# Kernel tuning notes

Measured on AMD Instinct MI355X. Metric: run time of the kernel, lower is better.

## Reference

```python
import jax, jax.numpy as jnp
import numpy as np

N, F, H, C, E = 100000, 128, 128, 40, 1600000


def setup_inputs() -> dict:
    key = jax.random.key(0)
    ks = jax.random.split(key, 8)
    x = jax.random.normal(ks[0], (N, F), dtype=jnp.float32)
    edge_index = jax.random.randint(ks[1], (2, E), 0, N, dtype=jnp.int64)
    s = 0.05
    return {
        "x": x,
        "edge_index": edge_index,
        "eps1": jnp.float32(0.0),
        "w1": jax.random.normal(ks[2], (F, H), dtype=jnp.float32) * s,
        "b1": jnp.zeros((H,), jnp.float32),
        "w2": jax.random.normal(ks[3], (H, H), dtype=jnp.float32) * s,
        "b2": jnp.zeros((H,), jnp.float32),
        "eps2": jnp.float32(0.0),
        "w3": jax.random.normal(ks[4], (H, H), dtype=jnp.float32) * s,
        "b3": jnp.zeros((H,), jnp.float32),
        "w4": jax.random.normal(ks[5], (H, C), dtype=jnp.float32) * s,
        "b4": jnp.zeros((C,), jnp.float32),
    }


def _gin_aggregate(h, src, dst, eps, n):
    # sum_{j -> i} h_j  +  (1+eps) * h_i
    agg = jax.ops.segment_sum(h[src], dst, num_segments=n)
    return (1.0 + eps) * h + agg


def reference(x, edge_index, eps1, w1, b1, w2, b2, eps2, w3, b3, w4, b4):
    src, dst = edge_index[0], edge_index[1]
    n = x.shape[0]
    # conv1: GINConv with MLP = Lin-ReLU-Lin-ReLU
    h = _gin_aggregate(x, src, dst, eps1, n)
    h = jax.nn.relu(h @ w1 + b1)
    h = jax.nn.relu(h @ w2 + b2)
    h = jax.nn.relu(h)  # outer F.relu (idempotent, kept for faithfulness)
    # dropout: identity in eval mode
    # conv2: GINConv with MLP = Lin-ReLU-Lin
    h2 = _gin_aggregate(h, src, dst, eps2, n)
    h2 = jax.nn.relu(h2 @ w3 + b3)
    h2 = h2 @ w4 + b4
    return jax.nn.log_softmax(h2, axis=1)
```

## Files before the change

kernel.cpp:

```cpp
#include <hip/hip_runtime.h>
#include <hip/hip_fp16.h>
#include <math.h>

constexpr int F = 128;
constexpr int C = 40;
constexpr int LDH = 136;
constexpr int BSHIFT = 8;
constexpr int BSIZE = 1 << BSHIFT;
constexpr int CHUNK = 8192;

typedef __attribute__((ext_vector_type(8))) _Float16 half8;
typedef __attribute__((ext_vector_type(4))) float float4v;


__global__ __launch_bounds__(256) void coarse_hist_kernel(const int* __restrict__ dst, int E, int NB,
                                                          int* __restrict__ coarse_count) {
    __shared__ int hist[512];
    int t = threadIdx.x;
    int c0 = blockIdx.x * CHUNK;
    int cend = min(c0 + CHUNK, E);
    for (int i = t; i < NB; i += 256) hist[i] = 0;
    __syncthreads();
    for (int i = c0 + t; i < cend; i += 256)
        atomicAdd(&hist[dst[i] >> BSHIFT], 1);
    __syncthreads();
    for (int i = t; i < NB; i += 256)
        if (hist[i]) atomicAdd(&coarse_count[i], hist[i]);
}

__global__ __launch_bounds__(512) void coarse_scan_kernel(const int* __restrict__ coarse_count,
                                                          int NB, int E,
                                                          int* __restrict__ coarse_start,
                                                          int* __restrict__ bucket_pos,
                                                          int* __restrict__ row_start, int N) {
    __shared__ int tmp[512];
    int t = threadIdx.x;
    int v = (t < NB) ? coarse_count[t] : 0;
    tmp[t] = v;
    __syncthreads();
    for (int d = 1; d < 512; d <<= 1) {
        int add = (t >= d) ? tmp[t - d] : 0;
        __syncthreads();
        tmp[t] += add;
        __syncthreads();
    }
    if (t < NB) {
        int ex = tmp[t] - v;
        coarse_start[t] = ex;
        bucket_pos[t] = ex;
    }
    if (t == 0) {
        coarse_start[NB] = E;
        row_start[N] = E;
    }
}

__global__ __launch_bounds__(256) void bucket_scatter_a_kernel(
        const int* __restrict__ src, const int* __restrict__ dst, int E, int NB,
        int* __restrict__ bucket_pos, unsigned* __restrict__ pairs) {
    __shared__ int hist[512];
    __shared__ int base[512];
    int t = threadIdx.x;
    int c0 = blockIdx.x * CHUNK;
    int cend = min(c0 + CHUNK, E);
    for (int i = t; i < NB; i += 256) hist[i] = 0;
    __syncthreads();
    for (int i = c0 + t; i < cend; i += 256)
        atomicAdd(&hist[dst[i] >> BSHIFT], 1);
    __syncthreads();
    for (int i = t; i < NB; i += 256) {
        int h = hist[i];
        base[i] = (h > 0) ? atomicAdd(&bucket_pos[i], h) : 0;
        hist[i] = 0;
    }
    __syncthreads();
    for (int i = c0 + t; i < cend; i += 256) {
        int d = dst[i];
        int b = d >> BSHIFT;
        int p = base[b] + atomicAdd(&hist[b], 1);
        pairs[p] = ((unsigned)(d & (BSIZE - 1)) << 24) | (unsigned)src[i];
    }
}

__global__ __launch_bounds__(256) void bucket_sort_kernel(const unsigned* __restrict__ pairs,
                                                          const int* __restrict__ coarse_start,
                                                          int N, int* __restrict__ row_start,
                                                          int* __restrict__ src_sorted) {
    __shared__ int hist[256];
    __shared__ int tmp[256];
    int b = blockIdx.x, t = threadIdx.x;
    int base = b << BSHIFT;
    int start = coarse_start[b];
    int end = coarse_start[b + 1];
    hist[t] = 0;
    __syncthreads();
    for (int i = start + t; i < end; i += 256)
        atomicAdd(&hist[pairs[i] >> 24], 1);
    __syncthreads();
    int v = hist[t];
    tmp[t] = v;
    __syncthreads();
    for (int d = 1; d < 256; d <<= 1) {
        int add = (t >= d) ? tmp[t - d] : 0;
        __syncthreads();
        tmp[t] += add;
        __syncthreads();
    }
    int ex = start + tmp[t] - v;
    if (base + t < N) row_start[base + t] = ex;
    hist[t] = ex;
    __syncthreads();
    for (int i = start + t; i < end; i += 256) {
        unsigned u = pairs[i];
        int p = atomicAdd(&hist[u >> 24], 1);
        src_sorted[p] = (int)(u & 0x00FFFFFFu);
    }
}


__global__ void conv_f16_kernel(const float* __restrict__ in, __half* __restrict__ out, int n4,
                                int* __restrict__ coarse_count, int NB) {
    int i = blockIdx.x * blockDim.x + threadIdx.x;
    if (blockIdx.x == 0) {
        for (int j = threadIdx.x; j < NB; j += 256) coarse_count[j] = 0;
    }
    if (i >= n4) return;
    float4 v = ((const float4*)in)[i];
    __half2 a = __floats2half2_rn(v.x, v.y);
    __half2 b = __floats2half2_rn(v.z, v.w);
    uint2 o;
    o.x = __builtin_bit_cast(unsigned, a);
    o.y = __builtin_bit_cast(unsigned, b);
    ((uint2*)out)[i] = o;
}


__global__ __launch_bounds__(256) void prep_weights_kernel(
        const float* __restrict__ w1, const float* __restrict__ w2,
        const float* __restrict__ w3, const float* __restrict__ w4,
        __half* __restrict__ w1t, __half* __restrict__ w2t,
        __half* __restrict__ w3t, __half* __restrict__ w4t) {
    __shared__ float lds[128 * 128];
    const float* in; __half* outp; int Nin, Npad;
    switch (blockIdx.x) {
        case 0:  in = w1; outp = w1t; Nin = 128; Npad = 128; break;
        case 1:  in = w2; outp = w2t; Nin = 128; Npad = 128; break;
        case 2:  in = w3; outp = w3t; Nin = 128; Npad = 128; break;
        default: in = w4; outp = w4t; Nin = 40;  Npad = 48;  break;
    }
    int t = threadIdx.x;
    int nf4 = 128 * Nin / 4;
    for (int i = t; i < nf4; i += 256)
        ((float4*)lds)[i] = ((const float4*)in)[i];
    __syncthreads();
    int total = Npad * 64;
    for (int i = t; i < total; i += 256) {
        int n = i >> 6, k2 = (i & 63) * 2;
        float lo = 0.f, hi = 0.f;
        if (n < Nin) {
            lo = lds[k2 * Nin + n];
            hi = lds[(k2 + 1) * Nin + n];
        }
        __half2 h = __floats2half2_rn(lo, hi);
        ((unsigned*)outp)[i] = __builtin_bit_cast(unsigned, h);
    }
}


__global__ __launch_bounds__(256) void agg_f16_kernel(const __half* __restrict__ feat,
        const int* __restrict__ row_start, const int* __restrict__ src_sorted,
        const float* __restrict__ eps_ptr, __half* __restrict__ out, int N) {
    int wid = (int)((blockIdx.x * blockDim.x + threadIdx.x) >> 6);
    int lane = threadIdx.x & 63;
    if (wid >= N) return;
    int q = lane >> 4, l16 = lane & 15;
    int s = row_start[wid], e = row_start[wid + 1];
    __half2 A0, A1, A2, A3, B0, B1, B2, B3;
    A0 = A1 = A2 = A3 = B0 = B1 = B2 = B3 = __builtin_bit_cast(__half2, 0u);
    int i = s + q;
    for (; i + 4 < e; i += 8) {
        int sv0 = src_sorted[i];
        int sv1 = src_sorted[i + 4];
        uint4 u0 = *(((const uint4*)(feat + (size_t)sv0 * F)) + l16);
        uint4 u1 = *(((const uint4*)(feat + (size_t)sv1 * F)) + l16);
        A0 = __hadd2(A0, __builtin_bit_cast(__half2, u0.x));
        A1 = __hadd2(A1, __builtin_bit_cast(__half2, u0.y));
        A2 = __hadd2(A2, __builtin_bit_cast(__half2, u0.z));
        A3 = __hadd2(A3, __builtin_bit_cast(__half2, u0.w));
        B0 = __hadd2(B0, __builtin_bit_cast(__half2, u1.x));
        B1 = __hadd2(B1, __builtin_bit_cast(__half2, u1.y));
        B2 = __hadd2(B2, __builtin_bit_cast(__half2, u1.z));
        B3 = __hadd2(B3, __builtin_bit_cast(__half2, u1.w));
    }
    if (i < e) {
        int sv = src_sorted[i];
        uint4 u = *(((const uint4*)(feat + (size_t)sv * F)) + l16);
        A0 = __hadd2(A0, __builtin_bit_cast(__half2, u.x));
        A1 = __hadd2(A1, __builtin_bit_cast(__half2, u.y));
        A2 = __hadd2(A2, __builtin_bit_cast(__half2, u.z));
        A3 = __hadd2(A3, __builtin_bit_cast(__half2, u.w));
    }
    float a[8];
    {
        float2 fa, fb;
        fa = __half22float2(A0); fb = __half22float2(B0); a[0] = fa.x + fb.x; a[1] = fa.y + fb.y;
        fa = __half22float2(A1); fb = __half22float2(B1); a[2] = fa.x + fb.x; a[3] = fa.y + fb.y;
        fa = __half22float2(A2); fb = __half22float2(B2); a[4] = fa.x + fb.x; a[5] = fa.y + fb.y;
        fa = __half22float2(A3); fb = __half22float2(B3); a[6] = fa.x + fb.x; a[7] = fa.y + fb.y;
    }
#pragma unroll
    for (int j = 0; j < 8; ++j) {
        a[j] += __shfl_xor(a[j], 16);
        a[j] += __shfl_xor(a[j], 32);
    }
    if (q == 0) {
        float ep1 = 1.0f + *eps_ptr;
        uint4 u = *(((const uint4*)(feat + (size_t)wid * F)) + l16);
        float2 s0 = __half22float2(__builtin_bit_cast(__half2, u.x));
        float2 s1 = __half22float2(__builtin_bit_cast(__half2, u.y));
        float2 s2 = __half22float2(__builtin_bit_cast(__half2, u.z));
        float2 s3 = __half22float2(__builtin_bit_cast(__half2, u.w));
        a[0] = fmaf(ep1, s0.x, a[0]); a[1] = fmaf(ep1, s0.y, a[1]);
        a[2] = fmaf(ep1, s1.x, a[2]); a[3] = fmaf(ep1, s1.y, a[3]);
        a[4] = fmaf(ep1, s2.x, a[4]); a[5] = fmaf(ep1, s2.y, a[5]);
        a[6] = fmaf(ep1, s3.x, a[6]); a[7] = fmaf(ep1, s3.y, a[7]);
        uint4 ou;
        ou.x = __builtin_bit_cast(unsigned, __floats2half2_rn(a[0], a[1]));
        ou.y = __builtin_bit_cast(unsigned, __floats2half2_rn(a[2], a[3]));
        ou.z = __builtin_bit_cast(unsigned, __floats2half2_rn(a[4], a[5]));
        ou.w = __builtin_bit_cast(unsigned, __floats2half2_rn(a[6], a[7]));
        *(((uint4*)(out + (size_t)wid * F)) + l16) = ou;
    }
}


__global__ __launch_bounds__(256) void mlp1_mfma_kernel(const __half* __restrict__ A,
        const __half* __restrict__ w1t, const float* __restrict__ b1,
        const __half* __restrict__ w2t, const float* __restrict__ b2,
        __half* __restrict__ out, int N) {
    __shared__ __half ldsA[64 * LDH];
    __shared__ __half ldsW[128 * LDH];
    __shared__ float ldsB[256];
    int t = threadIdx.x;
    int wave = t >> 6, lane = t & 63, quad = lane >> 4, l16 = lane & 15;
    int br = blockIdx.x * 64;
    if (t < 128) ldsB[t] = b1[t];
    else         ldsB[t] = b2[t - 128];
    for (int i = t; i < 1024; i += 256) {
        int r = i >> 4, c = i & 15;
        int gr = br + r;
        uint4 v = make_uint4(0u, 0u, 0u, 0u);
        if (gr < N) v = *((const uint4*)(A + (size_t)gr * F + c * 8));
        *((uint4*)&ldsA[r * LDH + c * 8]) = v;
    }
    for (int i = t; i < 2048; i += 256) {
        int r = i >> 4, c = i & 15;
        *((uint4*)&ldsW[r * LDH + c * 8]) = *((const uint4*)(w1t + r * 128 + c * 8));
    }
    __syncthreads();

    int ct0 = wave * 2;
    float4v acc[4][2];
    float4v zero = {0.f, 0.f, 0.f, 0.f};
#pragma unroll
    for (int i = 0; i < 4; ++i)
#pragma unroll
        for (int j = 0; j < 2; ++j) acc[i][j] = zero;

#pragma unroll
    for (int ks = 0; ks < 4; ++ks) {
        half8 af[4], wf[2];
#pragma unroll
        for (int i = 0; i < 4; ++i)
            af[i] = *((const half8*)&ldsA[(i * 16 + l16) * LDH + ks * 32 + quad * 8]);
#pragma unroll
        for (int j = 0; j < 2; ++j)
            wf[j] = *((const half8*)&ldsW[((ct0 + j) * 16 + l16) * LDH + ks * 32 + quad * 8]);
#pragma unroll
        for (int i = 0; i < 4; ++i)
#pragma unroll
            for (int j = 0; j < 2; ++j)
                acc[i][j] = __builtin_amdgcn_mfma_f32_16x16x32_f16(wf[j], af[i], acc[i][j], 0, 0, 0);
    }
    __syncthreads();
#pragma unroll
    for (int j = 0; j < 2; ++j) {
        int c = ct0 + j;
        float4 bb = *((const float4*)&ldsB[c * 16 + quad * 4]);
#pragma unroll
        for (int i = 0; i < 4; ++i) {
            float v0 = acc[i][j][0] + bb.x; v0 = v0 > 0.f ? v0 : 0.f;
            float v1 = acc[i][j][1] + bb.y; v1 = v1 > 0.f ? v1 : 0.f;
            float v2 = acc[i][j][2] + bb.z; v2 = v2 > 0.f ? v2 : 0.f;
            float v3 = acc[i][j][3] + bb.w; v3 = v3 > 0.f ? v3 : 0.f;
            __half2 h0 = __floats2half2_rn(v0, v1);
            __half2 h1 = __floats2half2_rn(v2, v3);
            uint2 o;
            o.x = __builtin_bit_cast(unsigned, h0);
            o.y = __builtin_bit_cast(unsigned, h1);
            *((uint2*)&ldsA[(i * 16 + l16) * LDH + c * 16 + quad * 4]) = o;
        }
    }
    for (int i = t; i < 2048; i += 256) {
        int r = i >> 4, c = i & 15;
        *((uint4*)&ldsW[r * LDH + c * 8]) = *((const uint4*)(w2t + r * 128 + c * 8));
    }
    __syncthreads();

#pragma unroll
    for (int i = 0; i < 4; ++i)
#pragma unroll
        for (int j = 0; j < 2; ++j) acc[i][j] = zero;
#pragma unroll
    for (int ks = 0; ks < 4; ++ks) {
        half8 af[4], wf[2];
#pragma unroll
        for (int i = 0; i < 4; ++i)
            af[i] = *((const half8*)&ldsA[(i * 16 + l16) * LDH + ks * 32 + quad * 8]);
#pragma unroll
        for (int j = 0; j < 2; ++j)
            wf[j] = *((const half8*)&ldsW[((ct0 + j) * 16 + l16) * LDH + ks * 32 + quad * 8]);
#pragma unroll
        for (int i = 0; i < 4; ++i)
#pragma unroll
            for (int j = 0; j < 2; ++j)
                acc[i][j] = __builtin_amdgcn_mfma_f32_16x16x32_f16(wf[j], af[i], acc[i][j], 0, 0, 0);
    }
    __syncthreads();
#pragma unroll
    for (int j = 0; j < 2; ++j) {
        int c = ct0 + j;
        float4 bb = *((const float4*)&ldsB[128 + c * 16 + quad * 4]);
#pragma unroll
        for (int i = 0; i < 4; ++i) {
            float v0 = acc[i][j][0] + bb.x; v0 = v0 > 0.f ? v0 : 0.f;
            float v1 = acc[i][j][1] + bb.y; v1 = v1 > 0.f ? v1 : 0.f;
            float v2 = acc[i][j][2] + bb.z; v2 = v2 > 0.f ? v2 : 0.f;
            float v3 = acc[i][j][3] + bb.w; v3 = v3 > 0.f ? v3 : 0.f;
            __half2 h0 = __floats2half2_rn(v0, v1);
            __half2 h1 = __floats2half2_rn(v2, v3);
            uint2 o;
            o.x = __builtin_bit_cast(unsigned, h0);
            o.y = __builtin_bit_cast(unsigned, h1);
            *((uint2*)&ldsA[(i * 16 + l16) * LDH + c * 16 + quad * 4]) = o;
        }
    }
    __syncthreads();
    for (int i = t; i < 1024; i += 256) {
        int r = i >> 4, c = i & 15;
        int gr = br + r;
        if (gr < N)
            *((uint4*)(out + (size_t)gr * F + c * 8)) = *((const uint4*)&ldsA[r * LDH + c * 8]);
    }
}


__global__ __launch_bounds__(256) void mlp2_mfma_kernel(const __half* __restrict__ A,
        const __half* __restrict__ w3t, const float* __restrict__ b3,
        const __half* __restrict__ w4t, const float* __restrict__ b4,
        float* __restrict__ out, int N) {
    __shared__ __half ldsA[64 * LDH];
    __shared__ __half ldsW[128 * LDH];
    __shared__ float ldsB[176];
    int t = threadIdx.x;
    int wave = t >> 6, lane = t & 63, quad = lane >> 4, l16 = lane & 15;
    int br = blockIdx.x * 64;
    if (t < 128) ldsB[t] = b3[t];
    else if (t < 176) ldsB[t] = (t - 128 < C) ? b4[t - 128] : 0.f;
    for (int i = t; i < 1024; i += 256) {
        int r = i >> 4, c = i & 15;
        int gr = br + r;
        uint4 v = make_uint4(0u, 0u, 0u, 0u);
        if (gr < N) v = *((const uint4*)(A + (size_t)gr * F + c * 8));
        *((uint4*)&ldsA[r * LDH + c * 8]) = v;
    }
    for (int i = t; i < 2048; i += 256) {
        int r = i >> 4, c = i & 15;
        *((uint4*)&ldsW[r * LDH + c * 8]) = *((const uint4*)(w3t + r * 128 + c * 8));
    }
    __syncthreads();

    int ct0 = wave * 2;
    float4v acc[4][2];
    float4v zero = {0.f, 0.f, 0.f, 0.f};
#pragma unroll
    for (int i = 0; i < 4; ++i)
#pragma unroll
        for (int j = 0; j < 2; ++j) acc[i][j] = zero;
#pragma unroll
    for (int ks = 0; ks < 4; ++ks) {
        half8 af[4], wf[2];
#pragma unroll
        for (int i = 0; i < 4; ++i)
            af[i] = *((const half8*)&ldsA[(i * 16 + l16) * LDH + ks * 32 + quad * 8]);
#pragma unroll
        for (int j = 0; j < 2; ++j)
            wf[j] = *((const half8*)&ldsW[((ct0 + j) * 16 + l16) * LDH + ks * 32 + quad * 8]);
#pragma unroll
        for (int i = 0; i < 4; ++i)
#pragma unroll
            for (int j = 0; j < 2; ++j)
                acc[i][j] = __builtin_amdgcn_mfma_f32_16x16x32_f16(wf[j], af[i], acc[i][j], 0, 0, 0);
    }
    __syncthreads();
#pragma unroll
    for (int j = 0; j < 2; ++j) {
        int c = ct0 + j;
        float4 bb = *((const float4*)&ldsB[c * 16 + quad * 4]);
#pragma unroll
        for (int i = 0; i < 4; ++i) {
            float v0 = acc[i][j][0] + bb.x; v0 = v0 > 0.f ? v0 : 0.f;
            float v1 = acc[i][j][1] + bb.y; v1 = v1 > 0.f ? v1 : 0.f;
            float v2 = acc[i][j][2] + bb.z; v2 = v2 > 0.f ? v2 : 0.f;
            float v3 = acc[i][j][3] + bb.w; v3 = v3 > 0.f ? v3 : 0.f;
            __half2 h0 = __floats2half2_rn(v0, v1);
            __half2 h1 = __floats2half2_rn(v2, v3);
            uint2 o;
            o.x = __builtin_bit_cast(unsigned, h0);
            o.y = __builtin_bit_cast(unsigned, h1);
            *((uint2*)&ldsA[(i * 16 + l16) * LDH + c * 16 + quad * 4]) = o;
        }
    }
    for (int i = t; i < 768; i += 256) {
        int r = i >> 4, c = i & 15;
        *((uint4*)&ldsW[r * LDH + c * 8]) = *((const uint4*)(w4t + r * 128 + c * 8));
    }
    __syncthreads();

    float4v acc4[3];
#pragma unroll
    for (int c = 0; c < 3; ++c) acc4[c] = zero;
#pragma unroll
    for (int ks = 0; ks < 4; ++ks) {
        half8 af = *((const half8*)&ldsA[(wave * 16 + l16) * LDH + ks * 32 + quad * 8]);
#pragma unroll
        for (int c = 0; c < 3; ++c) {
            half8 wf = *((const half8*)&ldsW[(c * 16 + l16) * LDH + ks * 32 + quad * 8]);
            acc4[c] = __builtin_amdgcn_mfma_f32_16x16x32_f16(wf, af, acc4[c], 0, 0, 0);
        }
    }
    float lv[3][4];
#pragma unroll
    for (int c = 0; c < 3; ++c) {
        float4 bb = *((const float4*)&ldsB[128 + c * 16 + quad * 4]);
        lv[c][0] = acc4[c][0] + bb.x;
        lv[c][1] = acc4[c][1] + bb.y;
        lv[c][2] = acc4[c][2] + bb.z;
        lv[c][3] = acc4[c][3] + bb.w;
    }
    bool tile2ok = (quad < 2);
    float m = -1e30f;
#pragma unroll
    for (int c = 0; c < 3; ++c) {
        if (c == 2 && !tile2ok) continue;
#pragma unroll
        for (int r = 0; r < 4; ++r) m = fmaxf(m, lv[c][r]);
    }
    m = fmaxf(m, __shfl_xor(m, 16));
    m = fmaxf(m, __shfl_xor(m, 32));
    float ssum = 0.f;
#pragma unroll
    for (int c = 0; c < 3; ++c) {
        if (c == 2 && !tile2ok) continue;
#pragma unroll
        for (int r = 0; r < 4; ++r) ssum += __expf(lv[c][r] - m);
    }
    ssum += __shfl_xor(ssum, 16);
    ssum += __shfl_xor(ssum, 32);
    float L = m + __logf(ssum);
    int node = br + wave * 16 + l16;
    if (node < N) {
#pragma unroll
        for (int c = 0; c < 3; ++c) {
            if (c == 2 && !tile2ok) continue;
            float4 o = make_float4(lv[c][0] - L, lv[c][1] - L, lv[c][2] - L, lv[c][3] - L);
            *((float4*)(out + (size_t)node * C + c * 16 + quad * 4)) = o;
        }
    }
}


extern "C" void kernel_launch(void* const* d_in, const int* in_sizes, int n_in,
                              void* d_out, int out_size, void* d_ws, size_t ws_size,
                              hipStream_t stream) {
    const float* x    = (const float*)d_in[0];
    const int*   ei   = (const int*)d_in[1];
    const float* eps1 = (const float*)d_in[2];
    const float* w1   = (const float*)d_in[3];
    const float* b1   = (const float*)d_in[4];
    const float* w2   = (const float*)d_in[5];
    const float* b2   = (const float*)d_in[6];
    const float* eps2 = (const float*)d_in[7];
    const float* w3   = (const float*)d_in[8];
    const float* b3   = (const float*)d_in[9];
    const float* w4   = (const float*)d_in[10];
    const float* b4   = (const float*)d_in[11];
    float* out = (float*)d_out;

    int N = in_sizes[0] / F;
    int E = in_sizes[1] / 2;
    const int* src = ei;
    const int* dst = ei + E;

    int NB = (N + BSIZE - 1) >> BSHIFT;
    int BA = (E + CHUNK - 1) / CHUNK;

    __half* x_h  = (__half*)d_ws;
    __half* h0_h = x_h + (size_t)N * F;
    __half* h_h  = h0_h + (size_t)N * F;
    __half* w1t  = h_h + (size_t)N * F;
    __half* w2t  = w1t + 128 * 128;
    __half* w3t  = w2t + 128 * 128;
    __half* w4t  = w3t + 128 * 128;
    unsigned* pairs   = (unsigned*)(w4t + 48 * 128);
    int* row_start    = (int*)(pairs + E);
    int* src_sorted   = row_start + (N + 1);
    int* coarse_count = src_sorted + E;
    int* coarse_start = coarse_count + 512;
    int* bucket_pos   = coarse_start + 513;

    int n4 = N * F / 4;
    conv_f16_kernel<<<(n4 + 255) / 256, 256, 0, stream>>>(x, x_h, n4, coarse_count, NB);
    prep_weights_kernel<<<4, 256, 0, stream>>>(w1, w2, w3, w4, w1t, w2t, w3t, w4t);

    coarse_hist_kernel<<<BA, 256, 0, stream>>>(dst, E, NB, coarse_count);
    coarse_scan_kernel<<<1, 512, 0, stream>>>(coarse_count, NB, E, coarse_start, bucket_pos,
                                              row_start, N);
    bucket_scatter_a_kernel<<<BA, 256, 0, stream>>>(src, dst, E, NB, bucket_pos, pairs);
    bucket_sort_kernel<<<NB, 256, 0, stream>>>(pairs, coarse_start, N, row_start, src_sorted);

    agg_f16_kernel<<<(N + 3) / 4, 256, 0, stream>>>(x_h, row_start, src_sorted, eps1, h0_h, N);
    mlp1_mfma_kernel<<<(N + 63) / 64, 256, 0, stream>>>(h0_h, w1t, b1, w2t, b2, h_h, N);
    agg_f16_kernel<<<(N + 3) / 4, 256, 0, stream>>>(h_h, row_start, src_sorted, eps2, h0_h, N);
    mlp2_mfma_kernel<<<(N + 63) / 64, 256, 0, stream>>>(h0_h, w3t, b3, w4t, b4, out, N);
}
```

Baseline: 354.6 us.

## Merge prep kernels into one launch and deepen aggregation unroll

Three kernels (fp32-to-fp16 conversion of x, weight transpose, and the coarse destination histogram) become one kernel that picks its job from the block index. The coarse_count reset moves to a hipMemsetAsync. This cuts launch count and lets independent work run at the same time. Separately, the aggregation gather loop gets a 16-edge step with four accumulator sets, putting more loads in flight per lane at the cost of extra registers. Every block of the merged kernel now reserves the weight-transpose LDS buffer, which may lower occupancy for the conversion and histogram blocks.

```diff
diff --git a/kernel.cpp b/kernel.cpp
--- a/kernel.cpp
+++ b/kernel.cpp
@@ -13,11 +13,42 @@
 typedef __attribute__((ext_vector_type(4))) float float4v;
 
 
-__global__ __launch_bounds__(256) void coarse_hist_kernel(const int* __restrict__ dst, int E, int NB,
-                                                          int* __restrict__ coarse_count) {
+__device__ void prep_conv(const float* in, __half* out, int n4, int blk) {
+    int i = blk * 256 + threadIdx.x;
+    if (i >= n4) return;
+    float4 v = ((const float4*)in)[i];
+    __half2 a = __floats2half2_rn(v.x, v.y);
+    __half2 b = __floats2half2_rn(v.z, v.w);
+    uint2 o;
+    o.x = __builtin_bit_cast(unsigned, a);
+    o.y = __builtin_bit_cast(unsigned, b);
+    ((uint2*)out)[i] = o;
+}
+
+__device__ void prep_weight(const float* in, __half* outp, int Nin, int Npad) {
+    __shared__ float lds[128 * 128];
+    int t = threadIdx.x;
+    int nf4 = 128 * Nin / 4;
+    for (int i = t; i < nf4; i += 256)
+        ((float4*)lds)[i] = ((const float4*)in)[i];
+    __syncthreads();
+    int total = Npad * 64;
+    for (int i = t; i < total; i += 256) {
+        int n = i >> 6, k2 = (i & 63) * 2;
+        float lo = 0.f, hi = 0.f;
+        if (n < Nin) {
+            lo = lds[k2 * Nin + n];
+            hi = lds[(k2 + 1) * Nin + n];
+        }
+        __half2 h = __floats2half2_rn(lo, hi);
+        ((unsigned*)outp)[i] = __builtin_bit_cast(unsigned, h);
+    }
+}
+
+__device__ void prep_hist(const int* dst, int E, int NB, int* coarse_count, int blk) {
     __shared__ int hist[512];
     int t = threadIdx.x;
-    int c0 = blockIdx.x * CHUNK;
+    int c0 = blk * CHUNK;
     int cend = min(c0 + CHUNK, E);
     for (int i = t; i < NB; i += 256) hist[i] = 0;
     __syncthreads();
@@ -27,6 +58,29 @@
     for (int i = t; i < NB; i += 256)
         if (hist[i]) atomicAdd(&coarse_count[i], hist[i]);
 }
+
+__global__ __launch_bounds__(256) void prep_kernel(
+        const float* __restrict__ x, __half* __restrict__ x_h, int n4, int Bconv,
+        const float* __restrict__ w1, const float* __restrict__ w2,
+        const float* __restrict__ w3, const float* __restrict__ w4,
+        __half* __restrict__ w1t, __half* __restrict__ w2t,
+        __half* __restrict__ w3t, __half* __restrict__ w4t,
+        const int* __restrict__ dst, int E, int NB, int* __restrict__ coarse_count) {
+    int b = blockIdx.x;
+    if (b < Bconv) {
+        prep_conv(x, x_h, n4, b);
+    } else if (b < Bconv + 4) {
+        switch (b - Bconv) {
+            case 0: prep_weight(w1, w1t, 128, 128); break;
+            case 1: prep_weight(w2, w2t, 128, 128); break;
+            case 2: prep_weight(w3, w3t, 128, 128); break;
+            default: prep_weight(w4, w4t, 40, 48); break;
+        }
+    } else {
+        prep_hist(dst, E, NB, coarse_count, b - Bconv - 4);
+    }
+}
+
 
 __global__ __launch_bounds__(512) void coarse_scan_kernel(const int* __restrict__ coarse_count,
                                                           int NB, int E,
@@ -118,55 +172,6 @@
 }
 
 
-__global__ void conv_f16_kernel(const float* __restrict__ in, __half* __restrict__ out, int n4,
-                                int* __restrict__ coarse_count, int NB) {
-    int i = blockIdx.x * blockDim.x + threadIdx.x;
-    if (blockIdx.x == 0) {
-        for (int j = threadIdx.x; j < NB; j += 256) coarse_count[j] = 0;
-    }
-    if (i >= n4) return;
-    float4 v = ((const float4*)in)[i];
-    __half2 a = __floats2half2_rn(v.x, v.y);
-    __half2 b = __floats2half2_rn(v.z, v.w);
-    uint2 o;
-    o.x = __builtin_bit_cast(unsigned, a);
-    o.y = __builtin_bit_cast(unsigned, b);
-    ((uint2*)out)[i] = o;
-}
-
-
-__global__ __launch_bounds__(256) void prep_weights_kernel(
-        const float* __restrict__ w1, const float* __restrict__ w2,
-        const float* __restrict__ w3, const float* __restrict__ w4,
-        __half* __restrict__ w1t, __half* __restrict__ w2t,
-        __half* __restrict__ w3t, __half* __restrict__ w4t) {
-    __shared__ float lds[128 * 128];
-    const float* in; __half* outp; int Nin, Npad;
-    switch (blockIdx.x) {
-        case 0:  in = w1; outp = w1t; Nin = 128; Npad = 128; break;
-        case 1:  in = w2; outp = w2t; Nin = 128; Npad = 128; break;
-        case 2:  in = w3; outp = w3t; Nin = 128; Npad = 128; break;
-        default: in = w4; outp = w4t; Nin = 40;  Npad = 48;  break;
-    }
-    int t = threadIdx.x;
-    int nf4 = 128 * Nin / 4;
-    for (int i = t; i < nf4; i += 256)
-        ((float4*)lds)[i] = ((const float4*)in)[i];
-    __syncthreads();
-    int total = Npad * 64;
-    for (int i = t; i < total; i += 256) {
-        int n = i >> 6, k2 = (i & 63) * 2;
-        float lo = 0.f, hi = 0.f;
-        if (n < Nin) {
-            lo = lds[k2 * Nin + n];
-            hi = lds[(k2 + 1) * Nin + n];
-        }
-        __half2 h = __floats2half2_rn(lo, hi);
-        ((unsigned*)outp)[i] = __builtin_bit_cast(unsigned, h);
-    }
-}
-
-
 __global__ __launch_bounds__(256) void agg_f16_kernel(const __half* __restrict__ feat,
         const int* __restrict__ row_start, const int* __restrict__ src_sorted,
         const float* __restrict__ eps_ptr, __half* __restrict__ out, int N) {
@@ -176,8 +181,36 @@
     int q = lane >> 4, l16 = lane & 15;
     int s = row_start[wid], e = row_start[wid + 1];
     __half2 A0, A1, A2, A3, B0, B1, B2, B3;
+    __half2 C0, C1, C2, C3, D0, D1, D2, D3;
     A0 = A1 = A2 = A3 = B0 = B1 = B2 = B3 = __builtin_bit_cast(__half2, 0u);
+    C0 = C1 = C2 = C3 = D0 = D1 = D2 = D3 = __builtin_bit_cast(__half2, 0u);
     int i = s + q;
+    for (; i + 12 < e; i += 16) {
+        int sv0 = src_sorted[i];
+        int sv1 = src_sorted[i + 4];
+        int sv2 = src_sorted[i + 8];
+        int sv3 = src_sorted[i + 12];
+        uint4 u0 = *(((const uint4*)(feat + (size_t)sv0 * F)) + l16);
+        uint4 u1 = *(((const uint4*)(feat + (size_t)sv1 * F)) + l16);
+        uint4 u2 = *(((const uint4*)(feat + (size_t)sv2 * F)) + l16);
+        uint4 u3 = *(((const uint4*)(feat + (size_t)sv3 * F)) + l16);
+        A0 = __hadd2(A0, __builtin_bit_cast(__half2, u0.x));
+        A1 = __hadd2(A1, __builtin_bit_cast(__half2, u0.y));
+        A2 = __hadd2(A2, __builtin_bit_cast(__half2, u0.z));
+        A3 = __hadd2(A3, __builtin_bit_cast(__half2, u0.w));
+        B0 = __hadd2(B0, __builtin_bit_cast(__half2, u1.x));
+        B1 = __hadd2(B1, __builtin_bit_cast(__half2, u1.y));
+        B2 = __hadd2(B2, __builtin_bit_cast(__half2, u1.z));
+        B3 = __hadd2(B3, __builtin_bit_cast(__half2, u1.w));
+        C0 = __hadd2(C0, __builtin_bit_cast(__half2, u2.x));
+        C1 = __hadd2(C1, __builtin_bit_cast(__half2, u2.y));
+        C2 = __hadd2(C2, __builtin_bit_cast(__half2, u2.z));
+        C3 = __hadd2(C3, __builtin_bit_cast(__half2, u2.w));
+        D0 = __hadd2(D0, __builtin_bit_cast(__half2, u3.x));
+        D1 = __hadd2(D1, __builtin_bit_cast(__half2, u3.y));
+        D2 = __hadd2(D2, __builtin_bit_cast(__half2, u3.z));
+        D3 = __hadd2(D3, __builtin_bit_cast(__half2, u3.w));
+    }
     for (; i + 4 < e; i += 8) {
         int sv0 = src_sorted[i];
         int sv1 = src_sorted[i + 4];
@@ -202,11 +235,19 @@
     }
     float a[8];
     {
-        float2 fa, fb;
-        fa = __half22float2(A0); fb = __half22float2(B0); a[0] = fa.x + fb.x; a[1] = fa.y + fb.y;
-        fa = __half22float2(A1); fb = __half22float2(B1); a[2] = fa.x + fb.x; a[3] = fa.y + fb.y;
-        fa = __half22float2(A2); fb = __half22float2(B2); a[4] = fa.x + fb.x; a[5] = fa.y + fb.y;
-        fa = __half22float2(A3); fb = __half22float2(B3); a[6] = fa.x + fb.x; a[7] = fa.y + fb.y;
+        float2 fa, fb, fc, fd;
+        fa = __half22float2(A0); fb = __half22float2(B0);
+        fc = __half22float2(C0); fd = __half22float2(D0);
+        a[0] = (fa.x + fb.x) + (fc.x + fd.x); a[1] = (fa.y + fb.y) + (fc.y + fd.y);
+        fa = __half22float2(A1); fb = __half22float2(B1);
+        fc = __half22float2(C1); fd = __half22float2(D1);
+        a[2] = (fa.x + fb.x) + (fc.x + fd.x); a[3] = (fa.y + fb.y) + (fc.y + fd.y);
+        fa = __half22float2(A2); fb = __half22float2(B2);
+        fc = __half22float2(C2); fd = __half22float2(D2);
+        a[4] = (fa.x + fb.x) + (fc.x + fd.x); a[5] = (fa.y + fb.y) + (fc.y + fd.y);
+        fa = __half22float2(A3); fb = __half22float2(B3);
+        fc = __half22float2(C3); fd = __half22float2(D3);
+        a[6] = (fa.x + fb.x) + (fc.x + fd.x); a[7] = (fa.y + fb.y) + (fc.y + fd.y);
     }
 #pragma unroll
     for (int j = 0; j < 8; ++j) {
@@ -504,6 +545,8 @@
 
     int NB = (N + BSIZE - 1) >> BSHIFT;
     int BA = (E + CHUNK - 1) / CHUNK;
+    int n4 = N * F / 4;
+    int Bconv = (n4 + 255) / 256;
 
     __half* x_h  = (__half*)d_ws;
     __half* h0_h = x_h + (size_t)N * F;
@@ -519,11 +562,11 @@
     int* coarse_start = coarse_count + 512;
     int* bucket_pos   = coarse_start + 513;
 
-    int n4 = N * F / 4;
-    conv_f16_kernel<<<(n4 + 255) / 256, 256, 0, stream>>>(x, x_h, n4, coarse_count, NB);
-    prep_weights_kernel<<<4, 256, 0, stream>>>(w1, w2, w3, w4, w1t, w2t, w3t, w4t);
-
-    coarse_hist_kernel<<<BA, 256, 0, stream>>>(dst, E, NB, coarse_count);
+    hipMemsetAsync(coarse_count, 0, (size_t)NB * sizeof(int), stream);
+    prep_kernel<<<Bconv + 4 + BA, 256, 0, stream>>>(x, x_h, n4, Bconv,
+                                                    w1, w2, w3, w4, w1t, w2t, w3t, w4t,
+                                                    dst, E, NB, coarse_count);
+
     coarse_scan_kernel<<<1, 512, 0, stream>>>(coarse_count, NB, E, coarse_start, bucket_pos,
                                               row_start, N);
     bucket_scatter_a_kernel<<<BA, 256, 0, stream>>>(src, dst, E, NB, bucket_pos, pairs);
```

Measured after the change: 358.4 us. No clear change (+1.1%).

## Fuse input conversion, weight prep and histogram into one prep kernel

Applied to the files above, without the earlier changes.

Merges the fp16 conversion of x, the weight transpose/convert and the coarse destination histogram into one launch, dispatched by block index. The zeroing of coarse_count moves to a hipMemsetAsync. The edge CHUNK size drops from 8192 to 2048 so the histogram and scatter kernels run more blocks, and the aggregation kernel gets a launch_bounds occupancy hint. The fused kernel statically reserves the 64KB weight LDS buffer for every block, including the streaming conversion blocks, which may limit how many of them fit on a CU at once.

```diff
diff --git a/kernel.cpp b/kernel.cpp
--- a/kernel.cpp
+++ b/kernel.cpp
@@ -7,17 +7,48 @@
 constexpr int LDH = 136;
 constexpr int BSHIFT = 8;
 constexpr int BSIZE = 1 << BSHIFT;
-constexpr int CHUNK = 8192;
+constexpr int CHUNK = 2048;
 
 typedef __attribute__((ext_vector_type(8))) _Float16 half8;
 typedef __attribute__((ext_vector_type(4))) float float4v;
 
 
-__global__ __launch_bounds__(256) void coarse_hist_kernel(const int* __restrict__ dst, int E, int NB,
-                                                          int* __restrict__ coarse_count) {
+__device__ void prep_conv(const float* in, __half* out, int n4, int blk) {
+    int i = blk * 256 + threadIdx.x;
+    if (i >= n4) return;
+    float4 v = ((const float4*)in)[i];
+    __half2 a = __floats2half2_rn(v.x, v.y);
+    __half2 b = __floats2half2_rn(v.z, v.w);
+    uint2 o;
+    o.x = __builtin_bit_cast(unsigned, a);
+    o.y = __builtin_bit_cast(unsigned, b);
+    ((uint2*)out)[i] = o;
+}
+
+__device__ void prep_weight(const float* in, __half* outp, int Nin, int Npad) {
+    __shared__ float lds[128 * 128];
+    int t = threadIdx.x;
+    int nf4 = 128 * Nin / 4;
+    for (int i = t; i < nf4; i += 256)
+        ((float4*)lds)[i] = ((const float4*)in)[i];
+    __syncthreads();
+    int total = Npad * 64;
+    for (int i = t; i < total; i += 256) {
+        int n = i >> 6, k2 = (i & 63) * 2;
+        float lo = 0.f, hi = 0.f;
+        if (n < Nin) {
+            lo = lds[k2 * Nin + n];
+            hi = lds[(k2 + 1) * Nin + n];
+        }
+        __half2 h = __floats2half2_rn(lo, hi);
+        ((unsigned*)outp)[i] = __builtin_bit_cast(unsigned, h);
+    }
+}
+
+__device__ void prep_hist(const int* dst, int E, int NB, int* coarse_count, int blk) {
     __shared__ int hist[512];
     int t = threadIdx.x;
-    int c0 = blockIdx.x * CHUNK;
+    int c0 = blk * CHUNK;
     int cend = min(c0 + CHUNK, E);
     for (int i = t; i < NB; i += 256) hist[i] = 0;
     __syncthreads();
@@ -27,6 +58,29 @@
     for (int i = t; i < NB; i += 256)
         if (hist[i]) atomicAdd(&coarse_count[i], hist[i]);
 }
+
+__global__ __launch_bounds__(256) void prep_kernel(
+        const float* __restrict__ x, __half* __restrict__ x_h, int n4, int Bconv,
+        const float* __restrict__ w1, const float* __restrict__ w2,
+        const float* __restrict__ w3, const float* __restrict__ w4,
+        __half* __restrict__ w1t, __half* __restrict__ w2t,
+        __half* __restrict__ w3t, __half* __restrict__ w4t,
+        const int* __restrict__ dst, int E, int NB, int* __restrict__ coarse_count) {
+    int b = blockIdx.x;
+    if (b < Bconv) {
+        prep_conv(x, x_h, n4, b);
+    } else if (b < Bconv + 4) {
+        switch (b - Bconv) {
+            case 0: prep_weight(w1, w1t, 128, 128); break;
+            case 1: prep_weight(w2, w2t, 128, 128); break;
+            case 2: prep_weight(w3, w3t, 128, 128); break;
+            default: prep_weight(w4, w4t, 40, 48); break;
+        }
+    } else {
+        prep_hist(dst, E, NB, coarse_count, b - Bconv - 4);
+    }
+}
+
 
 __global__ __launch_bounds__(512) void coarse_scan_kernel(const int* __restrict__ coarse_count,
                                                           int NB, int E,
@@ -118,56 +172,7 @@
 }
 
 
-__global__ void conv_f16_kernel(const float* __restrict__ in, __half* __restrict__ out, int n4,
-                                int* __restrict__ coarse_count, int NB) {
-    int i = blockIdx.x * blockDim.x + threadIdx.x;
-    if (blockIdx.x == 0) {
-        for (int j = threadIdx.x; j < NB; j += 256) coarse_count[j] = 0;
-    }
-    if (i >= n4) return;
-    float4 v = ((const float4*)in)[i];
-    __half2 a = __floats2half2_rn(v.x, v.y);
-    __half2 b = __floats2half2_rn(v.z, v.w);
-    uint2 o;
-    o.x = __builtin_bit_cast(unsigned, a);
-    o.y = __builtin_bit_cast(unsigned, b);
-    ((uint2*)out)[i] = o;
-}
-
-
-__global__ __launch_bounds__(256) void prep_weights_kernel(
-        const float* __restrict__ w1, const float* __restrict__ w2,
-        const float* __restrict__ w3, const float* __restrict__ w4,
-        __half* __restrict__ w1t, __half* __restrict__ w2t,
-        __half* __restrict__ w3t, __half* __restrict__ w4t) {
-    __shared__ float lds[128 * 128];
-    const float* in; __half* outp; int Nin, Npad;
-    switch (blockIdx.x) {
-        case 0:  in = w1; outp = w1t; Nin = 128; Npad = 128; break;
-        case 1:  in = w2; outp = w2t; Nin = 128; Npad = 128; break;
-        case 2:  in = w3; outp = w3t; Nin = 128; Npad = 128; break;
-        default: in = w4; outp = w4t; Nin = 40;  Npad = 48;  break;
-    }
-    int t = threadIdx.x;
-    int nf4 = 128 * Nin / 4;
-    for (int i = t; i < nf4; i += 256)
-        ((float4*)lds)[i] = ((const float4*)in)[i];
-    __syncthreads();
-    int total = Npad * 64;
-    for (int i = t; i < total; i += 256) {
-        int n = i >> 6, k2 = (i & 63) * 2;
-        float lo = 0.f, hi = 0.f;
-        if (n < Nin) {
-            lo = lds[k2 * Nin + n];
-            hi = lds[(k2 + 1) * Nin + n];
-        }
-        __half2 h = __floats2half2_rn(lo, hi);
-        ((unsigned*)outp)[i] = __builtin_bit_cast(unsigned, h);
-    }
-}
-
-
-__global__ __launch_bounds__(256) void agg_f16_kernel(const __half* __restrict__ feat,
+__global__ __launch_bounds__(256, 8) void agg_f16_kernel(const __half* __restrict__ feat,
         const int* __restrict__ row_start, const int* __restrict__ src_sorted,
         const float* __restrict__ eps_ptr, __half* __restrict__ out, int N) {
     int wid = (int)((blockIdx.x * blockDim.x + threadIdx.x) >> 6);
@@ -504,6 +509,8 @@
 
     int NB = (N + BSIZE - 1) >> BSHIFT;
     int BA = (E + CHUNK - 1) / CHUNK;
+    int n4 = N * F / 4;
+    int Bconv = (n4 + 255) / 256;
 
     __half* x_h  = (__half*)d_ws;
     __half* h0_h = x_h + (size_t)N * F;
@@ -519,11 +526,11 @@
     int* coarse_start = coarse_count + 512;
     int* bucket_pos   = coarse_start + 513;
 
-    int n4 = N * F / 4;
-    conv_f16_kernel<<<(n4 + 255) / 256, 256, 0, stream>>>(x, x_h, n4, coarse_count, NB);
-    prep_weights_kernel<<<4, 256, 0, stream>>>(w1, w2, w3, w4, w1t, w2t, w3t, w4t);
-
-    coarse_hist_kernel<<<BA, 256, 0, stream>>>(dst, E, NB, coarse_count);
+    hipMemsetAsync(coarse_count, 0, (size_t)NB * sizeof(int), stream);
+    prep_kernel<<<Bconv + 4 + BA, 256, 0, stream>>>(x, x_h, n4, Bconv,
+                                                    w1, w2, w3, w4, w1t, w2t, w3t, w4t,
+                                                    dst, E, NB, coarse_count);
+
     coarse_scan_kernel<<<1, 512, 0, stream>>>(coarse_count, NB, E, coarse_start, bucket_pos,
                                               row_start, N);
     bucket_scatter_a_kernel<<<BA, 256, 0, stream>>>(src, dst, E, NB, bucket_pos, pairs);
```

After: 380.2 us. 7.2% more time.
